# Performance work log

Measured on AMD Instinct MI355X. Metric: run time of the kernel, lower is better.

Reference implementation:

```python
import jax, jax.numpy as jnp
import numpy as np

ORDER = 2  # kernel_size


def setup_inputs() -> dict:
    key = jax.random.key(0)
    ks = jax.random.split(key, 8)
    B, F, N, T, H = 8, 1, 1024, 128, 64
    c_in = (ORDER * 2 + 1) * (2 * F + H)  # 330
    x = jax.random.normal(ks[0], (B, F, N, T), jnp.float32)
    mask = jax.random.randint(ks[1], (B, F, N, T), 0, 2).astype(jnp.bool_)
    adj = jax.random.uniform(ks[2], (N, N), jnp.float32)
    Wr = jax.random.normal(ks[3], (H, c_in), jnp.float32) * 0.05
    Wu = jax.random.normal(ks[4], (H, c_in), jnp.float32) * 0.05
    Wc = jax.random.normal(ks[5], (H, c_in), jnp.float32) * 0.05
    Wout = jax.random.normal(ks[6], (F, H), jnp.float32) * 0.05
    return {"x": x, "mask": mask, "adj": adj,
            "Wr": Wr, "br": jnp.zeros((H,), jnp.float32),
            "Wu": Wu, "bu": jnp.zeros((H,), jnp.float32),
            "Wc": Wc, "bc": jnp.zeros((H,), jnp.float32),
            "Wout": Wout, "bout": jnp.zeros((F,), jnp.float32)}


def reference(x, mask, adj, Wr, br, Wu, bu, Wc, bc, Wout, bout):
    # compute_support: forward/backward row-normalized diffusion matrices
    sup_f = adj / (adj.sum(1, keepdims=True) + 1e-8)
    adj_t = adj.T
    sup_b = adj_t / (adj_t.sum(1, keepdims=True) + 1e-8)
    supports = (sup_f, sup_b)

    def sconv(z, W, b):  # SpatialConvOrderK, z: [B,C,N]
        outs = [z]
        for a in supports:
            z1 = z
            for _ in range(ORDER):
                z1 = jnp.einsum('bcv,wv->bcw', z1, a)
                outs.append(z1)
        zc = jnp.concatenate(outs, axis=1)  # [B, 5*C, N]
        return jnp.einsum('bcn,oc->bon', zc, W) + b[None, :, None]

    def cell(inp, h):  # GCGRUCell
        xh = jnp.concatenate([inp, h], axis=1)
        r = jax.nn.sigmoid(sconv(xh, Wr, br))
        u = jax.nn.sigmoid(sconv(xh, Wu, bu))
        c = jnp.tanh(sconv(jnp.concatenate([inp, r * h], axis=1), Wc, bc))
        return u * h + (1.0 - u) * c

    B, F, N, T = x.shape
    H = Wout.shape[1]
    h0 = jnp.zeros((B, H, N), x.dtype)  # n_nodes=None -> zero init
    xs = jnp.moveaxis(x, -1, 0)    # [T,B,F,N]
    ms = jnp.moveaxis(mask, -1, 0)

    def step(h, xm):
        x_s, m_s = xm
        x_hat = jnp.einsum('bhn,oh->bon', h, Wout) + bout[None, :, None]
        state = h[None]  # n_layers=1 -> [L,B,H,N]
        x_in = jnp.where(m_s, x_s, x_hat)
        inp = jnp.concatenate([x_in, m_s.astype(x_s.dtype)], axis=1)
        return cell(inp, h), (x_hat, state)

    _, (preds, states) = jax.lax.scan(step, h0, (xs, ms))
    predictions = jnp.moveaxis(preds, 0, -1)  # [B,F,N,T]
    states = jnp.moveaxis(states, 0, -1)      # [L,B,H,N,T]
    return predictions, states
```

## Files before the change

kernel.cpp:

```cpp
#include <hip/hip_runtime.h>
#include <math.h>


typedef unsigned short u16;
typedef unsigned int u32;
typedef short bf16x8 __attribute__((ext_vector_type(8)));
typedef float f32x4 __attribute__((ext_vector_type(4)));

#define MFMA16(a, b, c) __builtin_amdgcn_mfma_f32_16x16x32_bf16((a), (b), (c), 0, 0, 0)

#define Bz 8
#define Nn 1024
#define Tt 128
#define Hh 64
#define KC 416
#define CP 80

static __device__ __forceinline__ u16 f2b(float f) {
  u32 u = __float_as_uint(f);
  u = (u + 0x7FFFu + ((u >> 16) & 1u)) >> 16;
  return (u16)u;
}
static __device__ __forceinline__ float b2f(u16 s) { return __uint_as_float(((u32)s) << 16); }
static __device__ __forceinline__ bf16x8 ld8(const u16* p) { return *reinterpret_cast<const bf16x8*>(p); }
static __device__ __forceinline__ void st2f(u16* p, float a, float b) {
  *reinterpret_cast<u32*>(p) = (u32)f2b(a) | ((u32)f2b(b) << 16);
}
static __device__ __forceinline__ void st2u(u16* p, u16 a, u16 b) {
  *reinterpret_cast<u32*>(p) = (u32)a | ((u32)b << 16);
}
static __device__ __forceinline__ float sigm(float x) { return 1.f / (1.f + __expf(-x)); }
static __device__ __forceinline__ float tanh_f(float x) {
  x = fminf(fmaxf(x, -15.f), 15.f);
  float e = __expf(2.f * x);
  return (e - 1.f) / (e + 1.f);
}

__global__ __launch_bounds__(256) void ksums(const float* adj, float* rinv, float* cinv) {
  int id = blockIdx.x * 256 + threadIdx.x;
  if (id < 1024) {
    int w = id;
    float s = 0.f;
    for (int v = 0; v < 1024; ++v) s += adj[v * 1024 + w];
    cinv[w] = 1.f / (s + 1e-8f);
  } else {
    int w = id - 1024;
    float s = 0.f;
    for (int v = 0; v < 1024; ++v) s += adj[w * 1024 + v];
    rinv[w] = 1.f / (s + 1e-8f);
  }
}

__global__ __launch_bounds__(256) void kmakeops(const float* adj, const float* rinv, const float* cinv,
                                                u16* Aops, u16* supft, u16* supbt) {
  int idx = blockIdx.x * 256 + threadIdx.x;
  int w = idx >> 10, v = idx & 1023;
  float a = adj[idx];
  u16 f = f2b(a * rinv[w]);
  u16 bb = f2b(a * cinv[v]);
  Aops[idx] = f;
  supft[v * 1024 + w] = f;
  supbt[idx] = bb;
  Aops[2 * 1048576 + v * 1024 + w] = bb;
}

__global__ __launch_bounds__(256) void kA2(u16* Aops, const u16* supft, const u16* supbt) {
  int wg = blockIdx.x;
  int o2 = wg & 1, mt = (wg >> 1) & 7, ntt = (wg >> 4) & 7;
  const u16* Ab = Aops + (o2 ? 2 * 1048576 : 0);
  const u16* Bb = o2 ? supbt : supft;
  u16* Ob = Aops + (o2 ? 3 * 1048576 : 1048576);
  int tid = threadIdx.x, wave = tid >> 6, lane = tid & 63, l15 = lane & 15, quad = lane >> 4;
  int mbase = mt * 128 + wave * 32;
  f32x4 acc[2][8];
#pragma unroll
  for (int m = 0; m < 2; ++m)
#pragma unroll
    for (int j = 0; j < 8; ++j) acc[m][j] = (f32x4){0.f, 0.f, 0.f, 0.f};
  for (int k = 0; k < 1024; k += 32) {
    int kq = k + quad * 8;
    bf16x8 av[2], bv[8];
#pragma unroll
    for (int m = 0; m < 2; ++m) av[m] = ld8(Ab + (mbase + m * 16 + l15) * 1024 + kq);
#pragma unroll
    for (int j = 0; j < 8; ++j) bv[j] = ld8(Bb + (ntt * 128 + j * 16 + l15) * 1024 + kq);
#pragma unroll
    for (int m = 0; m < 2; ++m)
#pragma unroll
      for (int j = 0; j < 8; ++j) acc[m][j] = MFMA16(av[m], bv[j], acc[m][j]);
  }
#pragma unroll
  for (int m = 0; m < 2; ++m)
#pragma unroll
    for (int j = 0; j < 8; ++j) {
      int v = ntt * 128 + j * 16 + l15;
#pragma unroll
      for (int i = 0; i < 4; ++i) {
        int w = mbase + m * 16 + quad * 4 + i;
        Ob[w * 1024 + v] = f2b(acc[m][j][i]);
      }
    }
}

__global__ __launch_bounds__(256) void kpackw(const float* Wr, const float* Wu, const float* Wc,
                                              u16* Wrup, u16* Wcp) {
  int idx = blockIdx.x * 256 + threadIdx.x;
  int r = idx / KC, k = idx % KC;
  float wv = 0.f;
  if (k < 396) {
    int c = (k < 66) ? k : (k - 66);
    if (r < 64) wv = Wr[r * 330 + c];
    else if (r < 128) wv = Wu[(r - 64) * 330 + c];
    else wv = Wc[(r - 128) * 330 + c];
  }
  if (r < 128) Wrup[r * KC + k] = f2b(wv);
  else Wcp[(r - 128) * KC + k] = f2b(wv);
}

__global__ __launch_bounds__(256) void kstep0(const float* x, const int* mask, const float* bout,
                                              float* h, float* states, float* preds,
                                              u16* xh, u16* xc, u16* zct, u16* yct) {
  int idx = blockIdx.x * 256 + threadIdx.x;
  int b = idx >> 16, o = (idx >> 10) & 63, n = idx & 1023;
  int hidx = (b * 64 + o) * 1024 + n;
  h[hidx] = 0.f;
  states[hidx * 128] = 0.f;
  xh[(b * CP + 2 + o) * 1024 + n] = 0;
  zct[(b * 1024 + n) * KC + 2 + o] = 0;
  zct[(b * 1024 + n) * KC + 68 + o] = 0;
  if (o == 0) {
    int xi = (b * 1024 + n) * 128;
    float xhat = bout[0];
    int mv = mask[xi];
    float xin = mv ? x[xi] : xhat;
    preds[xi] = xhat;
    u16 hi = f2b(xin), lo = f2b(xin - b2f(hi));
    xh[(b * CP + 0) * 1024 + n] = hi;
    xh[(b * CP + 1) * 1024 + n] = f2b((float)mv);
    u16* zr = zct + (b * 1024 + n) * KC;
    zr[0] = hi; zr[1] = f2b((float)mv); zr[66] = lo; zr[67] = 0;
  } else if (o == 1) {
    for (int j = 66; j < 80; ++j) {
      xh[(b * CP + j) * 1024 + n] = 0;
      xc[(b * CP + j) * 1024 + n] = 0;
    }
    u16* zr = zct + (b * 1024 + n) * KC;
    u16* yr = yct + (b * 1024 + n) * KC;
    for (int j = 396; j < KC; ++j) { zr[j] = 0; yr[j] = 0; }
  }
}

__global__ __launch_bounds__(256) void kdiff(const u16* __restrict__ Zin, const u16* __restrict__ Aops,
                                             u16* __restrict__ outT) {
  int wg = blockIdx.x;
  int nth = wg & 1, op = (wg >> 1) & 3, ntl = (wg >> 3) & 3, b = (wg >> 5) & 7;
  int nt = nth * 4 + ntl;
  int tid = threadIdx.x, wave = tid >> 6, lane = tid & 63, l15 = lane & 15, quad = lane >> 4;
  const u16* Zb = Zin + b * CP * 1024;
  const u16* Ab = Aops + op * 1048576;
  int colbase = nt * 128 + wave * 32;
  f32x4 acc[5][2];
#pragma unroll
  for (int m = 0; m < 5; ++m)
#pragma unroll
    for (int j = 0; j < 2; ++j) acc[m][j] = (f32x4){0.f, 0.f, 0.f, 0.f};
  for (int k = 0; k < 1024; k += 32) {
    int kq = k + quad * 8;
    bf16x8 av[5], bv[2];
#pragma unroll
    for (int m = 0; m < 5; ++m) av[m] = ld8(Zb + (m * 16 + l15) * 1024 + kq);
#pragma unroll
    for (int j = 0; j < 2; ++j) bv[j] = ld8(Ab + (colbase + j * 16 + l15) * 1024 + kq);
#pragma unroll
    for (int m = 0; m < 5; ++m)
#pragma unroll
      for (int j = 0; j < 2; ++j) acc[m][j] = MFMA16(av[m], bv[j], acc[m][j]);
  }
  int cbase = 132 + op * 66;
#pragma unroll
  for (int j = 0; j < 2; ++j) {
    int w = colbase + j * 16 + l15;
    u16* orow = outT + (b * 1024 + w) * KC + cbase;
#pragma unroll
    for (int m = 0; m < 5; ++m) {
      int c0 = m * 16 + quad * 4;
      if (c0 < 64) {
        st2f(orow + c0, acc[m][j][0], acc[m][j][1]);
        st2f(orow + c0 + 2, acc[m][j][2], acc[m][j][3]);
      } else if (c0 == 64) {
        st2f(orow + 64, acc[m][j][0], acc[m][j][1]);
      }
    }
  }
}

__global__ __launch_bounds__(256) void kconv_ru(const u16* __restrict__ zct, const u16* __restrict__ Wrup,
                                                const float* br, const float* bu,
                                                const float* __restrict__ h, float* __restrict__ ubuf,
                                                u16* __restrict__ xc, u16* __restrict__ yct) {
  int wg = blockIdx.x;
  int b = wg >> 5, nt = wg & 31;
  int tid = threadIdx.x, wave = tid >> 6, lane = tid & 63, l15 = lane & 15, quad = lane >> 4;
  int obase = wave * 32;
  f32x4 acc[2][2];
#pragma unroll
  for (int m = 0; m < 2; ++m)
#pragma unroll
    for (int j = 0; j < 2; ++j) acc[m][j] = (f32x4){0.f, 0.f, 0.f, 0.f};
  for (int k = 0; k < KC; k += 32) {
    int kq = k + quad * 8;
    bf16x8 av[2], bv[2];
#pragma unroll
    for (int m = 0; m < 2; ++m) av[m] = ld8(Wrup + (obase + m * 16 + l15) * KC + kq);
#pragma unroll
    for (int j = 0; j < 2; ++j) bv[j] = ld8(zct + ((b * 1024 + nt * 32 + j * 16 + l15) * KC + kq));
#pragma unroll
    for (int m = 0; m < 2; ++m)
#pragma unroll
      for (int j = 0; j < 2; ++j) acc[m][j] = MFMA16(av[m], bv[j], acc[m][j]);
  }
#pragma unroll
  for (int m = 0; m < 2; ++m)
#pragma unroll
    for (int j = 0; j < 2; ++j) {
      int o0 = obase + m * 16 + quad * 4;
      int n = nt * 32 + j * 16 + l15;
      if (o0 < 64) {
        u16 hi[4], lo[4];
#pragma unroll
        for (int i = 0; i < 4; ++i) {
          float s = sigm(acc[m][j][i] + br[o0 + i]);
          float rh = s * h[(b * 64 + o0 + i) * 1024 + n];
          hi[i] = f2b(rh);
          lo[i] = f2b(rh - b2f(hi[i]));
          xc[(b * CP + 2 + o0 + i) * 1024 + n] = hi[i];
        }
        u16* yr = yct + (b * 1024 + n) * KC;
        st2u(yr + 2 + o0, hi[0], hi[1]);
        st2u(yr + 4 + o0, hi[2], hi[3]);
        st2u(yr + 68 + o0, lo[0], lo[1]);
        st2u(yr + 70 + o0, lo[2], lo[3]);
      } else {
#pragma unroll
        for (int i = 0; i < 4; ++i)
          ubuf[(b * 64 + o0 - 64 + i) * 1024 + n] = sigm(acc[m][j][i] + bu[o0 - 64 + i]);
      }
    }
  if (tid < 32) {
    int n = nt * 32 + tid;
    const u16* zr = zct + (b * 1024 + n) * KC;
    u16* yr = yct + (b * 1024 + n) * KC;
    yr[0] = zr[0]; yr[1] = zr[1]; yr[66] = zr[66]; yr[67] = zr[67];
    xc[(b * CP + 0) * 1024 + n] = zr[0];
    xc[(b * CP + 1) * 1024 + n] = zr[1];
  }
}

__global__ __launch_bounds__(256) void kconv_c(const u16* __restrict__ yct, const u16* __restrict__ Wcp,
                                               const float* bc, const float* __restrict__ ubuf,
                                               float* __restrict__ h, const float* __restrict__ x,
                                               const int* __restrict__ mask, const float* Wout,
                                               const float* bout, float* __restrict__ preds,
                                               float* __restrict__ states, u16* __restrict__ xh,
                                               u16* __restrict__ zct, int t) {
  __shared__ float lds[64 * 65];
  int wg = blockIdx.x;
  int b = wg >> 4, nt = wg & 15;
  int tid = threadIdx.x, wave = tid >> 6, lane = tid & 63, l15 = lane & 15, quad = lane >> 4;
  int nl = wave * 16 + l15;
  int n = nt * 64 + nl;
  f32x4 acc[4];
#pragma unroll
  for (int m = 0; m < 4; ++m) acc[m] = (f32x4){0.f, 0.f, 0.f, 0.f};
  for (int k = 0; k < KC; k += 32) {
    int kq = k + quad * 8;
    bf16x8 bv = ld8(yct + (b * 1024 + n) * KC + kq);
#pragma unroll
    for (int m = 0; m < 4; ++m) {
      bf16x8 av = ld8(Wcp + (m * 16 + l15) * KC + kq);
      acc[m] = MFMA16(av, bv, acc[m]);
    }
  }
  int t1 = t + 1;
#pragma unroll
  for (int m = 0; m < 4; ++m) {
    int o0 = m * 16 + quad * 4;
    u16 hi[4], lo[4];
#pragma unroll
    for (int i = 0; i < 4; ++i) {
      int o = o0 + i;
      float c = tanh_f(acc[m][i] + bc[o]);
      int idx = (b * 64 + o) * 1024 + n;
      float u = ubuf[idx], hp = h[idx];
      float hn = u * hp + (1.f - u) * c;
      h[idx] = hn;
      lds[o * 65 + nl] = hn;
      hi[i] = f2b(hn);
      lo[i] = f2b(hn - b2f(hi[i]));
      if (t1 < Tt) {
        states[idx * 128 + t1] = hn;
        xh[(b * CP + 2 + o) * 1024 + n] = hi[i];
      }
    }
    if (t1 < Tt) {
      u16* zr = zct + (b * 1024 + n) * KC;
      st2u(zr + 2 + o0, hi[0], hi[1]);
      st2u(zr + 4 + o0, hi[2], hi[3]);
      st2u(zr + 68 + o0, lo[0], lo[1]);
      st2u(zr + 70 + o0, lo[2], lo[3]);
    }
  }
  __syncthreads();
  if (tid < 64 && t1 < Tt) {
    int nn = nt * 64 + tid;
    float xhat = bout[0];
    for (int o = 0; o < 64; ++o) xhat += Wout[o] * lds[o * 65 + tid];
    int xi = (b * 1024 + nn) * 128 + t1;
    int mv = mask[xi];
    float xin = mv ? x[xi] : xhat;
    preds[xi] = xhat;
    u16 hi = f2b(xin), lo = f2b(xin - b2f(hi));
    xh[(b * CP + 0) * 1024 + nn] = hi;
    xh[(b * CP + 1) * 1024 + nn] = f2b((float)mv);
    u16* zr = zct + (b * 1024 + nn) * KC;
    zr[0] = hi; zr[1] = f2b((float)mv); zr[66] = lo; zr[67] = 0;
  }
}

extern "C" void kernel_launch(void* const* d_in, const int* in_sizes, int n_in,
                              void* d_out, int out_size, void* d_ws, size_t ws_size,
                              hipStream_t stream) {
  const float* x = (const float*)d_in[0];
  const int* mask = (const int*)d_in[1];
  const float* adj = (const float*)d_in[2];
  const float* Wr = (const float*)d_in[3];
  const float* br = (const float*)d_in[4];
  const float* Wu = (const float*)d_in[5];
  const float* bu = (const float*)d_in[6];
  const float* Wc = (const float*)d_in[7];
  const float* bc = (const float*)d_in[8];
  const float* Wout = (const float*)d_in[9];
  const float* bout = (const float*)d_in[10];

  float* preds = (float*)d_out;
  float* states = preds + 8 * 1024 * 128;

  u16* Aops = (u16*)d_ws;
  u16* supft = Aops + 4 * 1048576;
  u16* supbt = supft + 1048576;
  float* rinv = (float*)(supbt + 1048576);
  float* cinv = rinv + 1024;
  u16* xh = (u16*)(cinv + 1024);
  u16* xc = xh + Bz * CP * 1024;
  u16* zct = xc + Bz * CP * 1024;
  u16* yct = zct + Bz * 1024 * KC;
  u16* Wrup = yct + Bz * 1024 * KC;
  u16* Wcp = Wrup + 128 * KC;
  float* ubuf = (float*)(Wcp + 64 * KC);
  float* h = ubuf + Bz * 64 * 1024;

  ksums<<<8, 256, 0, stream>>>(adj, rinv, cinv);
  kmakeops<<<4096, 256, 0, stream>>>(adj, rinv, cinv, Aops, supft, supbt);
  kA2<<<128, 256, 0, stream>>>(Aops, supft, supbt);
  kpackw<<<312, 256, 0, stream>>>(Wr, Wu, Wc, Wrup, Wcp);
  kstep0<<<2048, 256, 0, stream>>>(x, mask, bout, h, states, preds, xh, xc, zct, yct);

  for (int t = 0; t < Tt; ++t) {
    kdiff<<<256, 256, 0, stream>>>(xh, Aops, zct);
    kconv_ru<<<256, 256, 0, stream>>>(zct, Wrup, br, bu, h, ubuf, xc, yct);
    kdiff<<<256, 256, 0, stream>>>(xc, Aops, yct);
    kconv_c<<<128, 256, 0, stream>>>(yct, Wcp, bc, ubuf, h, x, mask, Wout, bout,
                                     preds, states, xh, zct, t);
  }
}
```

Baseline: 12.42 ms.

## Fuse diffusion GEMMs into gate-conv kernels via shared-memory staging

Merges each diffusion kernel with the following gate convolution (kdiff+kconv_ru into kphA, kdiff+kconv_c into kphB). Each 16-node tile computes the four diffusion outputs into LDS and then runs the weight GEMM from LDS, so the per-step launch count drops from four to two. The global z/y buffers shrink to a 136-wide stride that holds only the raw and hidden columns. In exchange, each block redundantly re-reads the full xh/xc operand for every 16-column tile, and the per-wave MFMA reuse is smaller.

```diff
diff --git a/kernel.cpp b/kernel.cpp
--- a/kernel.cpp
+++ b/kernel.cpp
@@ -10,10 +10,11 @@
 #define MFMA16(a, b, c) __builtin_amdgcn_mfma_f32_16x16x32_bf16((a), (b), (c), 0, 0, 0)
 
 #define Bz 8
-#define Nn 1024
 #define Tt 128
 #define Hh 64
 #define KC 416
+#define KD 136
+#define KL 424
 #define CP 80
 
 static __device__ __forceinline__ u16 f2b(float f) {
@@ -106,6 +107,7 @@
                                               u16* Wrup, u16* Wcp) {
   int idx = blockIdx.x * 256 + threadIdx.x;
   int r = idx / KC, k = idx % KC;
+  if (r >= 192) return;
   float wv = 0.f;
   if (k < 396) {
     int c = (k < 66) ? k : (k - 66);
@@ -119,15 +121,16 @@
 
 __global__ __launch_bounds__(256) void kstep0(const float* x, const int* mask, const float* bout,
                                               float* h, float* states, float* preds,
-                                              u16* xh, u16* xc, u16* zct, u16* yct) {
+                                              u16* xh, u16* xc, u16* zct) {
   int idx = blockIdx.x * 256 + threadIdx.x;
   int b = idx >> 16, o = (idx >> 10) & 63, n = idx & 1023;
   int hidx = (b * 64 + o) * 1024 + n;
   h[hidx] = 0.f;
-  states[hidx * 128] = 0.f;
+  states[(size_t)hidx * 128] = 0.f;
   xh[(b * CP + 2 + o) * 1024 + n] = 0;
-  zct[(b * 1024 + n) * KC + 2 + o] = 0;
-  zct[(b * 1024 + n) * KC + 68 + o] = 0;
+  u16* zr = zct + (size_t)(b * 1024 + n) * KD;
+  zr[2 + o] = 0;
+  zr[68 + o] = 0;
   if (o == 0) {
     int xi = (b * 1024 + n) * 128;
     float xhat = bout[0];
@@ -137,105 +140,88 @@
     u16 hi = f2b(xin), lo = f2b(xin - b2f(hi));
     xh[(b * CP + 0) * 1024 + n] = hi;
     xh[(b * CP + 1) * 1024 + n] = f2b((float)mv);
-    u16* zr = zct + (b * 1024 + n) * KC;
     zr[0] = hi; zr[1] = f2b((float)mv); zr[66] = lo; zr[67] = 0;
   } else if (o == 1) {
     for (int j = 66; j < 80; ++j) {
       xh[(b * CP + j) * 1024 + n] = 0;
       xc[(b * CP + j) * 1024 + n] = 0;
     }
-    u16* zr = zct + (b * 1024 + n) * KC;
-    u16* yr = yct + (b * 1024 + n) * KC;
-    for (int j = 396; j < KC; ++j) { zr[j] = 0; yr[j] = 0; }
-  }
-}
-
-__global__ __launch_bounds__(256) void kdiff(const u16* __restrict__ Zin, const u16* __restrict__ Aops,
-                                             u16* __restrict__ outT) {
+  }
+}
+
+__global__ __launch_bounds__(256) void kphA(const u16* __restrict__ xh, const u16* __restrict__ Aops,
+                                            const u16* __restrict__ zct, const u16* __restrict__ Wrup,
+                                            const float* br, const float* bu,
+                                            const float* __restrict__ h, float* __restrict__ ubuf,
+                                            u16* __restrict__ xc, u16* __restrict__ yct) {
+  __shared__ u16 zl[16][KL];
   int wg = blockIdx.x;
-  int nth = wg & 1, op = (wg >> 1) & 3, ntl = (wg >> 3) & 3, b = (wg >> 5) & 7;
-  int nt = nth * 4 + ntl;
+  int b = wg >> 6, nt = wg & 63;
   int tid = threadIdx.x, wave = tid >> 6, lane = tid & 63, l15 = lane & 15, quad = lane >> 4;
-  const u16* Zb = Zin + b * CP * 1024;
-  const u16* Ab = Aops + op * 1048576;
-  int colbase = nt * 128 + wave * 32;
-  f32x4 acc[5][2];
-#pragma unroll
-  for (int m = 0; m < 5; ++m)
-#pragma unroll
-    for (int j = 0; j < 2; ++j) acc[m][j] = (f32x4){0.f, 0.f, 0.f, 0.f};
-  for (int k = 0; k < 1024; k += 32) {
-    int kq = k + quad * 8;
-    bf16x8 av[5], bv[2];
-#pragma unroll
-    for (int m = 0; m < 5; ++m) av[m] = ld8(Zb + (m * 16 + l15) * 1024 + kq);
-#pragma unroll
-    for (int j = 0; j < 2; ++j) bv[j] = ld8(Ab + (colbase + j * 16 + l15) * 1024 + kq);
-#pragma unroll
-    for (int m = 0; m < 5; ++m)
-#pragma unroll
-      for (int j = 0; j < 2; ++j) acc[m][j] = MFMA16(av[m], bv[j], acc[m][j]);
-  }
-  int cbase = 132 + op * 66;
-#pragma unroll
-  for (int j = 0; j < 2; ++j) {
-    int w = colbase + j * 16 + l15;
-    u16* orow = outT + (b * 1024 + w) * KC + cbase;
+  for (int i = tid; i < 16 * 76; i += 256) {
+    int n = i / 76, c = i - n * 76;
+    u32* dst = (u32*)zl[n];
+    if (c < 66) dst[c] = ((const u32*)(zct + (size_t)(b * 1024 + nt * 16 + n) * KD))[c];
+    else dst[132 + c] = 0;
+  }
+  {
+    const u16* Zb = xh + b * CP * 1024;
+    const u16* Ab = Aops + (wave << 20);
+    int col = nt * 16 + l15;
+    f32x4 acc[5];
+#pragma unroll
+    for (int m = 0; m < 5; ++m) acc[m] = (f32x4){0.f, 0.f, 0.f, 0.f};
+    for (int k = 0; k < 1024; k += 32) {
+      int kq = k + quad * 8;
+      bf16x8 bv = ld8(Ab + col * 1024 + kq);
+      bf16x8 av[5];
+#pragma unroll
+      for (int m = 0; m < 5; ++m) av[m] = ld8(Zb + (m * 16 + l15) * 1024 + kq);
+#pragma unroll
+      for (int m = 0; m < 5; ++m) acc[m] = MFMA16(av[m], bv, acc[m]);
+    }
+    int cbase = 132 + wave * 66;
+    u16* orow = zl[l15] + cbase;
 #pragma unroll
     for (int m = 0; m < 5; ++m) {
       int c0 = m * 16 + quad * 4;
       if (c0 < 64) {
-        st2f(orow + c0, acc[m][j][0], acc[m][j][1]);
-        st2f(orow + c0 + 2, acc[m][j][2], acc[m][j][3]);
+        st2f(orow + c0, acc[m][0], acc[m][1]);
+        st2f(orow + c0 + 2, acc[m][2], acc[m][3]);
       } else if (c0 == 64) {
-        st2f(orow + 64, acc[m][j][0], acc[m][j][1]);
+        st2f(orow + 64, acc[m][0], acc[m][1]);
       }
     }
   }
-}
-
-__global__ __launch_bounds__(256) void kconv_ru(const u16* __restrict__ zct, const u16* __restrict__ Wrup,
-                                                const float* br, const float* bu,
-                                                const float* __restrict__ h, float* __restrict__ ubuf,
-                                                u16* __restrict__ xc, u16* __restrict__ yct) {
-  int wg = blockIdx.x;
-  int b = wg >> 5, nt = wg & 31;
-  int tid = threadIdx.x, wave = tid >> 6, lane = tid & 63, l15 = lane & 15, quad = lane >> 4;
-  int obase = wave * 32;
-  f32x4 acc[2][2];
-#pragma unroll
-  for (int m = 0; m < 2; ++m)
-#pragma unroll
-    for (int j = 0; j < 2; ++j) acc[m][j] = (f32x4){0.f, 0.f, 0.f, 0.f};
-  for (int k = 0; k < KC; k += 32) {
-    int kq = k + quad * 8;
-    bf16x8 av[2], bv[2];
-#pragma unroll
-    for (int m = 0; m < 2; ++m) av[m] = ld8(Wrup + (obase + m * 16 + l15) * KC + kq);
-#pragma unroll
-    for (int j = 0; j < 2; ++j) bv[j] = ld8(zct + ((b * 1024 + nt * 32 + j * 16 + l15) * KC + kq));
-#pragma unroll
-    for (int m = 0; m < 2; ++m)
-#pragma unroll
-      for (int j = 0; j < 2; ++j) acc[m][j] = MFMA16(av[m], bv[j], acc[m][j]);
-  }
-#pragma unroll
-  for (int m = 0; m < 2; ++m)
-#pragma unroll
-    for (int j = 0; j < 2; ++j) {
+  __syncthreads();
+  {
+    int obase = wave * 32;
+    f32x4 acc[2];
+    acc[0] = (f32x4){0.f, 0.f, 0.f, 0.f};
+    acc[1] = (f32x4){0.f, 0.f, 0.f, 0.f};
+    for (int k = 0; k < KC; k += 32) {
+      int kq = k + quad * 8;
+      bf16x8 bv = ld8(zl[l15] + kq);
+      bf16x8 av0 = ld8(Wrup + (obase + l15) * KC + kq);
+      bf16x8 av1 = ld8(Wrup + (obase + 16 + l15) * KC + kq);
+      acc[0] = MFMA16(av0, bv, acc[0]);
+      acc[1] = MFMA16(av1, bv, acc[1]);
+    }
+    int n = nt * 16 + l15;
+#pragma unroll
+    for (int m = 0; m < 2; ++m) {
       int o0 = obase + m * 16 + quad * 4;
-      int n = nt * 32 + j * 16 + l15;
       if (o0 < 64) {
         u16 hi[4], lo[4];
 #pragma unroll
         for (int i = 0; i < 4; ++i) {
-          float s = sigm(acc[m][j][i] + br[o0 + i]);
+          float s = sigm(acc[m][i] + br[o0 + i]);
           float rh = s * h[(b * 64 + o0 + i) * 1024 + n];
           hi[i] = f2b(rh);
           lo[i] = f2b(rh - b2f(hi[i]));
           xc[(b * CP + 2 + o0 + i) * 1024 + n] = hi[i];
         }
-        u16* yr = yct + (b * 1024 + n) * KC;
+        u16* yr = yct + (size_t)(b * 1024 + n) * KD;
         st2u(yr + 2 + o0, hi[0], hi[1]);
         st2u(yr + 4 + o0, hi[2], hi[3]);
         st2u(yr + 68 + o0, lo[0], lo[1]);
@@ -243,87 +229,118 @@
       } else {
 #pragma unroll
         for (int i = 0; i < 4; ++i)
-          ubuf[(b * 64 + o0 - 64 + i) * 1024 + n] = sigm(acc[m][j][i] + bu[o0 - 64 + i]);
+          ubuf[(b * 64 + o0 - 64 + i) * 1024 + n] = sigm(acc[m][i] + bu[o0 - 64 + i]);
       }
     }
-  if (tid < 32) {
-    int n = nt * 32 + tid;
-    const u16* zr = zct + (b * 1024 + n) * KC;
-    u16* yr = yct + (b * 1024 + n) * KC;
+  }
+  if (tid < 16) {
+    int n = nt * 16 + tid;
+    const u16* zr = zl[tid];
+    u16* yr = yct + (size_t)(b * 1024 + n) * KD;
     yr[0] = zr[0]; yr[1] = zr[1]; yr[66] = zr[66]; yr[67] = zr[67];
     xc[(b * CP + 0) * 1024 + n] = zr[0];
     xc[(b * CP + 1) * 1024 + n] = zr[1];
   }
 }
 
-__global__ __launch_bounds__(256) void kconv_c(const u16* __restrict__ yct, const u16* __restrict__ Wcp,
-                                               const float* bc, const float* __restrict__ ubuf,
-                                               float* __restrict__ h, const float* __restrict__ x,
-                                               const int* __restrict__ mask, const float* Wout,
-                                               const float* bout, float* __restrict__ preds,
-                                               float* __restrict__ states, u16* __restrict__ xh,
-                                               u16* __restrict__ zct, int t) {
-  __shared__ float lds[64 * 65];
+__global__ __launch_bounds__(256) void kphB(const u16* __restrict__ xc, const u16* __restrict__ Aops,
+                                            const u16* __restrict__ yct, const u16* __restrict__ Wcp,
+                                            const float* bc, const float* __restrict__ ubuf,
+                                            float* __restrict__ h, const float* __restrict__ x,
+                                            const int* __restrict__ mask, const float* Wout,
+                                            const float* bout, float* __restrict__ preds,
+                                            float* __restrict__ states, u16* __restrict__ xh,
+                                            u16* __restrict__ zct, int t) {
+  __shared__ u16 yl[16][KL];
+  __shared__ float hbuf[64][17];
   int wg = blockIdx.x;
-  int b = wg >> 4, nt = wg & 15;
+  int b = wg >> 6, nt = wg & 63;
   int tid = threadIdx.x, wave = tid >> 6, lane = tid & 63, l15 = lane & 15, quad = lane >> 4;
-  int nl = wave * 16 + l15;
-  int n = nt * 64 + nl;
-  f32x4 acc[4];
-#pragma unroll
-  for (int m = 0; m < 4; ++m) acc[m] = (f32x4){0.f, 0.f, 0.f, 0.f};
+  for (int i = tid; i < 16 * 76; i += 256) {
+    int n = i / 76, c = i - n * 76;
+    u32* dst = (u32*)yl[n];
+    if (c < 66) dst[c] = ((const u32*)(yct + (size_t)(b * 1024 + nt * 16 + n) * KD))[c];
+    else dst[132 + c] = 0;
+  }
+  {
+    const u16* Zb = xc + b * CP * 1024;
+    const u16* Ab = Aops + (wave << 20);
+    int col = nt * 16 + l15;
+    f32x4 acc[5];
+#pragma unroll
+    for (int m = 0; m < 5; ++m) acc[m] = (f32x4){0.f, 0.f, 0.f, 0.f};
+    for (int k = 0; k < 1024; k += 32) {
+      int kq = k + quad * 8;
+      bf16x8 bv = ld8(Ab + col * 1024 + kq);
+      bf16x8 av[5];
+#pragma unroll
+      for (int m = 0; m < 5; ++m) av[m] = ld8(Zb + (m * 16 + l15) * 1024 + kq);
+#pragma unroll
+      for (int m = 0; m < 5; ++m) acc[m] = MFMA16(av[m], bv, acc[m]);
+    }
+    int cbase = 132 + wave * 66;
+    u16* orow = yl[l15] + cbase;
+#pragma unroll
+    for (int m = 0; m < 5; ++m) {
+      int c0 = m * 16 + quad * 4;
+      if (c0 < 64) {
+        st2f(orow + c0, acc[m][0], acc[m][1]);
+        st2f(orow + c0 + 2, acc[m][2], acc[m][3]);
+      } else if (c0 == 64) {
+        st2f(orow + 64, acc[m][0], acc[m][1]);
+      }
+    }
+  }
+  __syncthreads();
+  f32x4 acc = (f32x4){0.f, 0.f, 0.f, 0.f};
   for (int k = 0; k < KC; k += 32) {
     int kq = k + quad * 8;
-    bf16x8 bv = ld8(yct + (b * 1024 + n) * KC + kq);
-#pragma unroll
-    for (int m = 0; m < 4; ++m) {
-      bf16x8 av = ld8(Wcp + (m * 16 + l15) * KC + kq);
-      acc[m] = MFMA16(av, bv, acc[m]);
-    }
+    bf16x8 bv = ld8(yl[l15] + kq);
+    bf16x8 av = ld8(Wcp + (wave * 16 + l15) * KC + kq);
+    acc = MFMA16(av, bv, acc);
   }
   int t1 = t + 1;
-#pragma unroll
-  for (int m = 0; m < 4; ++m) {
-    int o0 = m * 16 + quad * 4;
-    u16 hi[4], lo[4];
-#pragma unroll
-    for (int i = 0; i < 4; ++i) {
-      int o = o0 + i;
-      float c = tanh_f(acc[m][i] + bc[o]);
-      int idx = (b * 64 + o) * 1024 + n;
-      float u = ubuf[idx], hp = h[idx];
-      float hn = u * hp + (1.f - u) * c;
-      h[idx] = hn;
-      lds[o * 65 + nl] = hn;
-      hi[i] = f2b(hn);
-      lo[i] = f2b(hn - b2f(hi[i]));
-      if (t1 < Tt) {
-        states[idx * 128 + t1] = hn;
-        xh[(b * CP + 2 + o) * 1024 + n] = hi[i];
-      }
-    }
+  int n = nt * 16 + l15;
+  int o0 = wave * 16 + quad * 4;
+  u16 hi[4], lo[4];
+#pragma unroll
+  for (int i = 0; i < 4; ++i) {
+    int o = o0 + i;
+    float c = tanh_f(acc[i] + bc[o]);
+    int idx = (b * 64 + o) * 1024 + n;
+    float u = ubuf[idx], hp = h[idx];
+    float hn = u * hp + (1.f - u) * c;
+    h[idx] = hn;
+    hbuf[o][l15] = hn;
+    hi[i] = f2b(hn);
+    lo[i] = f2b(hn - b2f(hi[i]));
     if (t1 < Tt) {
-      u16* zr = zct + (b * 1024 + n) * KC;
-      st2u(zr + 2 + o0, hi[0], hi[1]);
-      st2u(zr + 4 + o0, hi[2], hi[3]);
-      st2u(zr + 68 + o0, lo[0], lo[1]);
-      st2u(zr + 70 + o0, lo[2], lo[3]);
-    }
+      states[(size_t)idx * 128 + t1] = hn;
+      xh[(b * CP + 2 + o) * 1024 + n] = hi[i];
+    }
+  }
+  if (t1 < Tt) {
+    u16* zr = zct + (size_t)(b * 1024 + n) * KD;
+    st2u(zr + 2 + o0, hi[0], hi[1]);
+    st2u(zr + 4 + o0, hi[2], hi[3]);
+    st2u(zr + 68 + o0, lo[0], lo[1]);
+    st2u(zr + 70 + o0, lo[2], lo[3]);
   }
   __syncthreads();
-  if (tid < 64 && t1 < Tt) {
-    int nn = nt * 64 + tid;
+  if (tid < 16 && t1 < Tt) {
+    int nn = nt * 16 + tid;
     float xhat = bout[0];
-    for (int o = 0; o < 64; ++o) xhat += Wout[o] * lds[o * 65 + tid];
+#pragma unroll
+    for (int o = 0; o < 64; ++o) xhat += Wout[o] * hbuf[o][tid];
     int xi = (b * 1024 + nn) * 128 + t1;
     int mv = mask[xi];
     float xin = mv ? x[xi] : xhat;
     preds[xi] = xhat;
-    u16 hi = f2b(xin), lo = f2b(xin - b2f(hi));
-    xh[(b * CP + 0) * 1024 + nn] = hi;
+    u16 hi2 = f2b(xin), lo2 = f2b(xin - b2f(hi2));
+    xh[(b * CP + 0) * 1024 + nn] = hi2;
     xh[(b * CP + 1) * 1024 + nn] = f2b((float)mv);
-    u16* zr = zct + (b * 1024 + nn) * KC;
-    zr[0] = hi; zr[1] = f2b((float)mv); zr[66] = lo; zr[67] = 0;
+    u16* zr = zct + (size_t)(b * 1024 + nn) * KD;
+    zr[0] = hi2; zr[1] = f2b((float)mv); zr[66] = lo2; zr[67] = 0;
   }
 }
 
@@ -353,8 +370,8 @@
   u16* xh = (u16*)(cinv + 1024);
   u16* xc = xh + Bz * CP * 1024;
   u16* zct = xc + Bz * CP * 1024;
-  u16* yct = zct + Bz * 1024 * KC;
-  u16* Wrup = yct + Bz * 1024 * KC;
+  u16* yct = zct + Bz * 1024 * KD;
+  u16* Wrup = yct + Bz * 1024 * KD;
   u16* Wcp = Wrup + 128 * KC;
   float* ubuf = (float*)(Wcp + 64 * KC);
   float* h = ubuf + Bz * 64 * 1024;
@@ -363,13 +380,11 @@
   kmakeops<<<4096, 256, 0, stream>>>(adj, rinv, cinv, Aops, supft, supbt);
   kA2<<<128, 256, 0, stream>>>(Aops, supft, supbt);
   kpackw<<<312, 256, 0, stream>>>(Wr, Wu, Wc, Wrup, Wcp);
-  kstep0<<<2048, 256, 0, stream>>>(x, mask, bout, h, states, preds, xh, xc, zct, yct);
+  kstep0<<<2048, 256, 0, stream>>>(x, mask, bout, h, states, preds, xh, xc, zct);
 
   for (int t = 0; t < Tt; ++t) {
-    kdiff<<<256, 256, 0, stream>>>(xh, Aops, zct);
-    kconv_ru<<<256, 256, 0, stream>>>(zct, Wrup, br, bu, h, ubuf, xc, yct);
-    kdiff<<<256, 256, 0, stream>>>(xc, Aops, yct);
-    kconv_c<<<128, 256, 0, stream>>>(yct, Wcp, bc, ubuf, h, x, mask, Wout, bout,
-                                     preds, states, xh, zct, t);
-  }
-}
+    kphA<<<512, 256, 0, stream>>>(xh, Aops, zct, Wrup, br, bu, h, ubuf, xc, yct);
+    kphB<<<512, 256, 0, stream>>>(xc, Aops, yct, Wcp, bc, ubuf, h, x, mask, Wout, bout,
+                                  preds, states, xh, zct, t);
+  }
+}
```

Result: slower. 14.07 ms (+13.3%).

## Fuse diffusion GEMM with gate convolution into two kernels per step via LDS

Applied to the files above, without the earlier changes.

Each timestep's diffusion matmul and following gate convolution are merged into one kernel: diffusion results are written into a shared-memory concat tile instead of the global zct/yct buffers, then consumed directly by the gate GEMM. This halves per-step launches from four to two and removes the global round-trip of the large transposed concat buffers. Both GEMMs use split-K across two wave halves with an LDS reduction. The hi/lo bf16 split channels now live as extra rows in xh/xc (CP raised to 148). The cost is heavier LDS use and extra syncs, which limits each block to one per CU.

```diff
diff --git a/kernel.cpp b/kernel.cpp
--- a/kernel.cpp
+++ b/kernel.cpp
@@ -10,11 +10,13 @@
 #define MFMA16(a, b, c) __builtin_amdgcn_mfma_f32_16x16x32_bf16((a), (b), (c), 0, 0, 0)
 
 #define Bz 8
-#define Nn 1024
 #define Tt 128
 #define Hh 64
 #define KC 416
-#define CP 80
+#define KL 424
+#define CP 148
+#define ZLB (32 * KL * 2)
+#define SCRB (4 * 64 * 44 * 4)
 
 static __device__ __forceinline__ u16 f2b(float f) {
   u32 u = __float_as_uint(f);
@@ -25,9 +27,6 @@
 static __device__ __forceinline__ bf16x8 ld8(const u16* p) { return *reinterpret_cast<const bf16x8*>(p); }
 static __device__ __forceinline__ void st2f(u16* p, float a, float b) {
   *reinterpret_cast<u32*>(p) = (u32)f2b(a) | ((u32)f2b(b) << 16);
-}
-static __device__ __forceinline__ void st2u(u16* p, u16 a, u16 b) {
-  *reinterpret_cast<u32*>(p) = (u32)a | ((u32)b << 16);
 }
 static __device__ __forceinline__ float sigm(float x) { return 1.f / (1.f + __expf(-x)); }
 static __device__ __forceinline__ float tanh_f(float x) {
@@ -106,6 +105,7 @@
                                               u16* Wrup, u16* Wcp) {
   int idx = blockIdx.x * 256 + threadIdx.x;
   int r = idx / KC, k = idx % KC;
+  if (r >= 192) return;
   float wv = 0.f;
   if (k < 396) {
     int c = (k < 66) ? k : (k - 66);
@@ -119,211 +119,309 @@
 
 __global__ __launch_bounds__(256) void kstep0(const float* x, const int* mask, const float* bout,
                                               float* h, float* states, float* preds,
-                                              u16* xh, u16* xc, u16* zct, u16* yct) {
-  int idx = blockIdx.x * 256 + threadIdx.x;
-  int b = idx >> 16, o = (idx >> 10) & 63, n = idx & 1023;
-  int hidx = (b * 64 + o) * 1024 + n;
-  h[hidx] = 0.f;
-  states[hidx * 128] = 0.f;
-  xh[(b * CP + 2 + o) * 1024 + n] = 0;
-  zct[(b * 1024 + n) * KC + 2 + o] = 0;
-  zct[(b * 1024 + n) * KC + 68 + o] = 0;
-  if (o == 0) {
-    int xi = (b * 1024 + n) * 128;
-    float xhat = bout[0];
-    int mv = mask[xi];
-    float xin = mv ? x[xi] : xhat;
-    preds[xi] = xhat;
-    u16 hi = f2b(xin), lo = f2b(xin - b2f(hi));
-    xh[(b * CP + 0) * 1024 + n] = hi;
-    xh[(b * CP + 1) * 1024 + n] = f2b((float)mv);
-    u16* zr = zct + (b * 1024 + n) * KC;
-    zr[0] = hi; zr[1] = f2b((float)mv); zr[66] = lo; zr[67] = 0;
-  } else if (o == 1) {
-    for (int j = 66; j < 80; ++j) {
-      xh[(b * CP + j) * 1024 + n] = 0;
-      xc[(b * CP + j) * 1024 + n] = 0;
-    }
-    u16* zr = zct + (b * 1024 + n) * KC;
-    u16* yr = yct + (b * 1024 + n) * KC;
-    for (int j = 396; j < KC; ++j) { zr[j] = 0; yr[j] = 0; }
-  }
-}
-
-__global__ __launch_bounds__(256) void kdiff(const u16* __restrict__ Zin, const u16* __restrict__ Aops,
-                                             u16* __restrict__ outT) {
+                                              u16* xh, u16* xc) {
   int wg = blockIdx.x;
-  int nth = wg & 1, op = (wg >> 1) & 3, ntl = (wg >> 3) & 3, b = (wg >> 5) & 7;
-  int nt = nth * 4 + ntl;
-  int tid = threadIdx.x, wave = tid >> 6, lane = tid & 63, l15 = lane & 15, quad = lane >> 4;
-  const u16* Zb = Zin + b * CP * 1024;
-  const u16* Ab = Aops + op * 1048576;
-  int colbase = nt * 128 + wave * 32;
-  f32x4 acc[5][2];
-#pragma unroll
-  for (int m = 0; m < 5; ++m)
-#pragma unroll
-    for (int j = 0; j < 2; ++j) acc[m][j] = (f32x4){0.f, 0.f, 0.f, 0.f};
-  for (int k = 0; k < 1024; k += 32) {
-    int kq = k + quad * 8;
-    bf16x8 av[5], bv[2];
-#pragma unroll
-    for (int m = 0; m < 5; ++m) av[m] = ld8(Zb + (m * 16 + l15) * 1024 + kq);
-#pragma unroll
-    for (int j = 0; j < 2; ++j) bv[j] = ld8(Ab + (colbase + j * 16 + l15) * 1024 + kq);
-#pragma unroll
-    for (int m = 0; m < 5; ++m)
-#pragma unroll
-      for (int j = 0; j < 2; ++j) acc[m][j] = MFMA16(av[m], bv[j], acc[m][j]);
-  }
-  int cbase = 132 + op * 66;
-#pragma unroll
-  for (int j = 0; j < 2; ++j) {
-    int w = colbase + j * 16 + l15;
-    u16* orow = outT + (b * 1024 + w) * KC + cbase;
-#pragma unroll
-    for (int m = 0; m < 5; ++m) {
-      int c0 = m * 16 + quad * 4;
-      if (c0 < 64) {
-        st2f(orow + c0, acc[m][j][0], acc[m][j][1]);
-        st2f(orow + c0 + 2, acc[m][j][2], acc[m][j][3]);
-      } else if (c0 == 64) {
-        st2f(orow + 64, acc[m][j][0], acc[m][j][1]);
-      }
-    }
-  }
-}
-
-__global__ __launch_bounds__(256) void kconv_ru(const u16* __restrict__ zct, const u16* __restrict__ Wrup,
-                                                const float* br, const float* bu,
-                                                const float* __restrict__ h, float* __restrict__ ubuf,
-                                                u16* __restrict__ xc, u16* __restrict__ yct) {
+  int b = wg / 148, row = wg - b * 148;
+  int n = threadIdx.x * 4;
+  for (int k = 0; k < 4; ++k, ++n) {
+    u16 xhv = 0;
+    if (row == 0 || row == 1 || row == 80) {
+      int xi = (b * 1024 + n) * 128;
+      int mv = mask[xi];
+      float xhat = bout[0];
+      float xin = mv ? x[xi] : xhat;
+      u16 hi = f2b(xin);
+      if (row == 0) { xhv = hi; preds[xi] = xhat; }
+      else if (row == 1) xhv = f2b((float)mv);
+      else xhv = f2b(xin - b2f(hi));
+    }
+    xh[(b * CP + row) * 1024 + n] = xhv;
+    xc[(b * CP + row) * 1024 + n] = 0;
+    if (row >= 2 && row < 66) {
+      int o = row - 2;
+      int idx = (b * 64 + o) * 1024 + n;
+      h[idx] = 0.f;
+      states[(size_t)idx * 128] = 0.f;
+    }
+  }
+}
+
+__global__ __launch_bounds__(512, 1) void kphA(const u16* __restrict__ xh, const u16* __restrict__ Aops,
+                                               const u16* __restrict__ Wrup,
+                                               const float* br, const float* bu,
+                                               const float* __restrict__ h, float* __restrict__ ubuf,
+                                               u16* __restrict__ xc) {
+  extern __shared__ char smem[];
+  u16 (*zl)[KL] = (u16(*)[KL])smem;
+  float* scr = (float*)(smem + ZLB);
   int wg = blockIdx.x;
   int b = wg >> 5, nt = wg & 31;
-  int tid = threadIdx.x, wave = tid >> 6, lane = tid & 63, l15 = lane & 15, quad = lane >> 4;
-  int obase = wave * 32;
-  f32x4 acc[2][2];
+  int n0 = nt * 32;
+  int tid = threadIdx.x, w = tid >> 6, lane = tid & 63, l15 = lane & 15, quad = lane >> 4;
+  int op = w & 3, kh = w >> 2;
+
+  for (int i = tid; i < 2112; i += 512) {
+    int ch = i >> 4, cp = i & 15;
+    int srow = ch < 66 ? ch : ch + 14;
+    u32 v = *(const u32*)(xh + (b * CP + srow) * 1024 + n0 + cp * 2);
+    zl[cp * 2][ch] = (u16)v;
+    zl[cp * 2 + 1][ch] = (u16)(v >> 16);
+    if (ch == 0 || ch == 1 || ch == 66 || ch == 67)
+      *(u32*)(xc + (b * CP + srow) * 1024 + n0 + cp * 2) = v;
+  }
+  for (int i = tid; i < 320; i += 512) {
+    int n = i / 10, c = i - n * 10;
+    ((u32*)zl[n])[198 + c] = 0;
+  }
+
+  f32x4 dacc[5][2];
+#pragma unroll
+  for (int m = 0; m < 5; ++m)
+#pragma unroll
+    for (int j = 0; j < 2; ++j) dacc[m][j] = (f32x4){0.f, 0.f, 0.f, 0.f};
+  {
+    const u16* Zb = xh + b * CP * 1024;
+    const u16* Ab = Aops + (op << 20);
+    int kbase = kh << 9;
+    for (int k = 0; k < 512; k += 32) {
+      int kq = kbase + k + quad * 8;
+      bf16x8 av[5], bv[2];
+#pragma unroll
+      for (int m = 0; m < 5; ++m) av[m] = ld8(Zb + (m * 16 + l15) * 1024 + kq);
+#pragma unroll
+      for (int j = 0; j < 2; ++j) bv[j] = ld8(Ab + (n0 + j * 16 + l15) * 1024 + kq);
+#pragma unroll
+      for (int m = 0; m < 5; ++m)
+#pragma unroll
+        for (int j = 0; j < 2; ++j) dacc[m][j] = MFMA16(av[m], bv[j], dacc[m][j]);
+    }
+  }
+  if (kh) {
+    f32x4* s = (f32x4*)(scr + (op * 64 + lane) * 44);
+#pragma unroll
+    for (int m = 0; m < 5; ++m)
+#pragma unroll
+      for (int j = 0; j < 2; ++j) s[m * 2 + j] = dacc[m][j];
+  }
+  __syncthreads();
+  if (!kh) {
+    f32x4* s = (f32x4*)(scr + (op * 64 + lane) * 44);
+    int cbase = 132 + op * 66;
+#pragma unroll
+    for (int m = 0; m < 5; ++m)
+#pragma unroll
+      for (int j = 0; j < 2; ++j) {
+        f32x4 a = dacc[m][j] + s[m * 2 + j];
+        u16* orow = zl[j * 16 + l15] + cbase;
+        int c0 = m * 16 + quad * 4;
+        if (c0 < 64) {
+          st2f(orow + c0, a[0], a[1]);
+          st2f(orow + c0 + 2, a[2], a[3]);
+        } else if (c0 == 64) {
+          st2f(orow + 64, a[0], a[1]);
+        }
+      }
+  }
+  __syncthreads();
+
+  int og = w & 3, obase = og * 32;
+  f32x4 cacc[2][2];
 #pragma unroll
   for (int m = 0; m < 2; ++m)
 #pragma unroll
-    for (int j = 0; j < 2; ++j) acc[m][j] = (f32x4){0.f, 0.f, 0.f, 0.f};
-  for (int k = 0; k < KC; k += 32) {
-    int kq = k + quad * 8;
-    bf16x8 av[2], bv[2];
-#pragma unroll
-    for (int m = 0; m < 2; ++m) av[m] = ld8(Wrup + (obase + m * 16 + l15) * KC + kq);
-#pragma unroll
-    for (int j = 0; j < 2; ++j) bv[j] = ld8(zct + ((b * 1024 + nt * 32 + j * 16 + l15) * KC + kq));
+    for (int j = 0; j < 2; ++j) cacc[m][j] = (f32x4){0.f, 0.f, 0.f, 0.f};
+  {
+    int k0 = kh ? 224 : 0, k1 = kh ? KC : 224;
+    for (int k = k0; k < k1; k += 32) {
+      int kq = k + quad * 8;
+      bf16x8 av[2], bv[2];
+#pragma unroll
+      for (int m = 0; m < 2; ++m) av[m] = ld8(Wrup + (obase + m * 16 + l15) * KC + kq);
+#pragma unroll
+      for (int j = 0; j < 2; ++j) bv[j] = ld8(zl[j * 16 + l15] + kq);
+#pragma unroll
+      for (int m = 0; m < 2; ++m)
+#pragma unroll
+        for (int j = 0; j < 2; ++j) cacc[m][j] = MFMA16(av[m], bv[j], cacc[m][j]);
+    }
+  }
+  if (kh) {
+    f32x4* s = (f32x4*)(scr + (og * 64 + lane) * 44);
 #pragma unroll
     for (int m = 0; m < 2; ++m)
 #pragma unroll
-      for (int j = 0; j < 2; ++j) acc[m][j] = MFMA16(av[m], bv[j], acc[m][j]);
-  }
-#pragma unroll
-  for (int m = 0; m < 2; ++m)
-#pragma unroll
-    for (int j = 0; j < 2; ++j) {
-      int o0 = obase + m * 16 + quad * 4;
-      int n = nt * 32 + j * 16 + l15;
-      if (o0 < 64) {
-        u16 hi[4], lo[4];
-#pragma unroll
-        for (int i = 0; i < 4; ++i) {
-          float s = sigm(acc[m][j][i] + br[o0 + i]);
-          float rh = s * h[(b * 64 + o0 + i) * 1024 + n];
-          hi[i] = f2b(rh);
-          lo[i] = f2b(rh - b2f(hi[i]));
-          xc[(b * CP + 2 + o0 + i) * 1024 + n] = hi[i];
+      for (int j = 0; j < 2; ++j) s[m * 2 + j] = cacc[m][j];
+  }
+  __syncthreads();
+  if (!kh) {
+    f32x4* s = (f32x4*)(scr + (og * 64 + lane) * 44);
+#pragma unroll
+    for (int m = 0; m < 2; ++m)
+#pragma unroll
+      for (int j = 0; j < 2; ++j) {
+        f32x4 a = cacc[m][j] + s[m * 2 + j];
+        int o0 = obase + m * 16 + quad * 4;
+        int n = n0 + j * 16 + l15;
+        if (o0 < 64) {
+#pragma unroll
+          for (int i = 0; i < 4; ++i) {
+            float sg = sigm(a[i] + br[o0 + i]);
+            float rh = sg * h[(b * 64 + o0 + i) * 1024 + n];
+            u16 hi = f2b(rh);
+            xc[(b * CP + 2 + o0 + i) * 1024 + n] = hi;
+            xc[(b * CP + 82 + o0 + i) * 1024 + n] = f2b(rh - b2f(hi));
+          }
+        } else {
+#pragma unroll
+          for (int i = 0; i < 4; ++i)
+            ubuf[(b * 64 + o0 - 64 + i) * 1024 + n] = sigm(a[i] + bu[o0 - 64 + i]);
         }
-        u16* yr = yct + (b * 1024 + n) * KC;
-        st2u(yr + 2 + o0, hi[0], hi[1]);
-        st2u(yr + 4 + o0, hi[2], hi[3]);
-        st2u(yr + 68 + o0, lo[0], lo[1]);
-        st2u(yr + 70 + o0, lo[2], lo[3]);
-      } else {
-#pragma unroll
-        for (int i = 0; i < 4; ++i)
-          ubuf[(b * 64 + o0 - 64 + i) * 1024 + n] = sigm(acc[m][j][i] + bu[o0 - 64 + i]);
       }
-    }
-  if (tid < 32) {
-    int n = nt * 32 + tid;
-    const u16* zr = zct + (b * 1024 + n) * KC;
-    u16* yr = yct + (b * 1024 + n) * KC;
-    yr[0] = zr[0]; yr[1] = zr[1]; yr[66] = zr[66]; yr[67] = zr[67];
-    xc[(b * CP + 0) * 1024 + n] = zr[0];
-    xc[(b * CP + 1) * 1024 + n] = zr[1];
-  }
-}
-
-__global__ __launch_bounds__(256) void kconv_c(const u16* __restrict__ yct, const u16* __restrict__ Wcp,
+  }
+}
+
+__global__ __launch_bounds__(512, 1) void kphB(const u16* __restrict__ xc, const u16* __restrict__ Aops,
+                                               const u16* __restrict__ Wcp,
                                                const float* bc, const float* __restrict__ ubuf,
                                                float* __restrict__ h, const float* __restrict__ x,
                                                const int* __restrict__ mask, const float* Wout,
                                                const float* bout, float* __restrict__ preds,
                                                float* __restrict__ states, u16* __restrict__ xh,
-                                               u16* __restrict__ zct, int t) {
-  __shared__ float lds[64 * 65];
+                                               int t) {
+  extern __shared__ char smem[];
+  u16 (*yl)[KL] = (u16(*)[KL])smem;
+  float* scr = (float*)(smem + ZLB);
+  float* hbuf = (float*)(smem + ZLB + SCRB);
   int wg = blockIdx.x;
-  int b = wg >> 4, nt = wg & 15;
-  int tid = threadIdx.x, wave = tid >> 6, lane = tid & 63, l15 = lane & 15, quad = lane >> 4;
-  int nl = wave * 16 + l15;
-  int n = nt * 64 + nl;
-  f32x4 acc[4];
-#pragma unroll
-  for (int m = 0; m < 4; ++m) acc[m] = (f32x4){0.f, 0.f, 0.f, 0.f};
-  for (int k = 0; k < KC; k += 32) {
-    int kq = k + quad * 8;
-    bf16x8 bv = ld8(yct + (b * 1024 + n) * KC + kq);
-#pragma unroll
-    for (int m = 0; m < 4; ++m) {
-      bf16x8 av = ld8(Wcp + (m * 16 + l15) * KC + kq);
-      acc[m] = MFMA16(av, bv, acc[m]);
-    }
-  }
+  int b = wg >> 5, nt = wg & 31;
+  int n0 = nt * 32;
+  int tid = threadIdx.x, w = tid >> 6, lane = tid & 63, l15 = lane & 15, quad = lane >> 4;
+  int op = w & 3, kh = w >> 2;
+
+  for (int i = tid; i < 2112; i += 512) {
+    int ch = i >> 4, cp = i & 15;
+    int srow = ch < 66 ? ch : ch + 14;
+    u32 v = *(const u32*)(xc + (b * CP + srow) * 1024 + n0 + cp * 2);
+    yl[cp * 2][ch] = (u16)v;
+    yl[cp * 2 + 1][ch] = (u16)(v >> 16);
+  }
+  for (int i = tid; i < 320; i += 512) {
+    int n = i / 10, c = i - n * 10;
+    ((u32*)yl[n])[198 + c] = 0;
+  }
+
+  f32x4 dacc[5][2];
+#pragma unroll
+  for (int m = 0; m < 5; ++m)
+#pragma unroll
+    for (int j = 0; j < 2; ++j) dacc[m][j] = (f32x4){0.f, 0.f, 0.f, 0.f};
+  {
+    const u16* Zb = xc + b * CP * 1024;
+    const u16* Ab = Aops + (op << 20);
+    int kbase = kh << 9;
+    for (int k = 0; k < 512; k += 32) {
+      int kq = kbase + k + quad * 8;
+      bf16x8 av[5], bv[2];
+#pragma unroll
+      for (int m = 0; m < 5; ++m) av[m] = ld8(Zb + (m * 16 + l15) * 1024 + kq);
+#pragma unroll
+      for (int j = 0; j < 2; ++j) bv[j] = ld8(Ab + (n0 + j * 16 + l15) * 1024 + kq);
+#pragma unroll
+      for (int m = 0; m < 5; ++m)
+#pragma unroll
+        for (int j = 0; j < 2; ++j) dacc[m][j] = MFMA16(av[m], bv[j], dacc[m][j]);
+    }
+  }
+  if (kh) {
+    f32x4* s = (f32x4*)(scr + (op * 64 + lane) * 44);
+#pragma unroll
+    for (int m = 0; m < 5; ++m)
+#pragma unroll
+      for (int j = 0; j < 2; ++j) s[m * 2 + j] = dacc[m][j];
+  }
+  __syncthreads();
+  if (!kh) {
+    f32x4* s = (f32x4*)(scr + (op * 64 + lane) * 44);
+    int cbase = 132 + op * 66;
+#pragma unroll
+    for (int m = 0; m < 5; ++m)
+#pragma unroll
+      for (int j = 0; j < 2; ++j) {
+        f32x4 a = dacc[m][j] + s[m * 2 + j];
+        u16* orow = yl[j * 16 + l15] + cbase;
+        int c0 = m * 16 + quad * 4;
+        if (c0 < 64) {
+          st2f(orow + c0, a[0], a[1]);
+          st2f(orow + c0 + 2, a[2], a[3]);
+        } else if (c0 == 64) {
+          st2f(orow + 64, a[0], a[1]);
+        }
+      }
+  }
+  __syncthreads();
+
+  int og = w & 1, jg = (w >> 1) & 1, task = w & 3;
+  int obase = og * 32;
+  f32x4 cacc[2];
+  cacc[0] = (f32x4){0.f, 0.f, 0.f, 0.f};
+  cacc[1] = (f32x4){0.f, 0.f, 0.f, 0.f};
+  {
+    int k0 = kh ? 224 : 0, k1 = kh ? KC : 224;
+    for (int k = k0; k < k1; k += 32) {
+      int kq = k + quad * 8;
+      bf16x8 bv = ld8(yl[jg * 16 + l15] + kq);
+      bf16x8 av0 = ld8(Wcp + (obase + l15) * KC + kq);
+      bf16x8 av1 = ld8(Wcp + (obase + 16 + l15) * KC + kq);
+      cacc[0] = MFMA16(av0, bv, cacc[0]);
+      cacc[1] = MFMA16(av1, bv, cacc[1]);
+    }
+  }
+  if (kh) {
+    f32x4* s = (f32x4*)(scr + (task * 64 + lane) * 44);
+    s[0] = cacc[0];
+    s[1] = cacc[1];
+  }
+  __syncthreads();
   int t1 = t + 1;
-#pragma unroll
-  for (int m = 0; m < 4; ++m) {
-    int o0 = m * 16 + quad * 4;
-    u16 hi[4], lo[4];
-#pragma unroll
-    for (int i = 0; i < 4; ++i) {
-      int o = o0 + i;
-      float c = tanh_f(acc[m][i] + bc[o]);
-      int idx = (b * 64 + o) * 1024 + n;
-      float u = ubuf[idx], hp = h[idx];
-      float hn = u * hp + (1.f - u) * c;
-      h[idx] = hn;
-      lds[o * 65 + nl] = hn;
-      hi[i] = f2b(hn);
-      lo[i] = f2b(hn - b2f(hi[i]));
-      if (t1 < Tt) {
-        states[idx * 128 + t1] = hn;
-        xh[(b * CP + 2 + o) * 1024 + n] = hi[i];
+  if (!kh) {
+    f32x4* s = (f32x4*)(scr + (task * 64 + lane) * 44);
+    int n = n0 + jg * 16 + l15, nloc = jg * 16 + l15;
+#pragma unroll
+    for (int m = 0; m < 2; ++m) {
+      f32x4 a = cacc[m] + s[m];
+      int o0 = obase + m * 16 + quad * 4;
+#pragma unroll
+      for (int i = 0; i < 4; ++i) {
+        int o = o0 + i;
+        float c = tanh_f(a[i] + bc[o]);
+        int idx = (b * 64 + o) * 1024 + n;
+        float u = ubuf[idx], hp = h[idx];
+        float hn = u * hp + (1.f - u) * c;
+        h[idx] = hn;
+        hbuf[o * 33 + nloc] = hn;
+        u16 hi = f2b(hn);
+        if (t1 < Tt) {
+          states[(size_t)idx * 128 + t1] = hn;
+          xh[(b * CP + 2 + o) * 1024 + n] = hi;
+          xh[(b * CP + 82 + o) * 1024 + n] = f2b(hn - b2f(hi));
+        }
       }
     }
-    if (t1 < Tt) {
-      u16* zr = zct + (b * 1024 + n) * KC;
-      st2u(zr + 2 + o0, hi[0], hi[1]);
-      st2u(zr + 4 + o0, hi[2], hi[3]);
-      st2u(zr + 68 + o0, lo[0], lo[1]);
-      st2u(zr + 70 + o0, lo[2], lo[3]);
-    }
-  }
-  __syncthreads();
-  if (tid < 64 && t1 < Tt) {
-    int nn = nt * 64 + tid;
+  }
+  __syncthreads();
+  if (tid < 32 && t1 < Tt) {
+    int nn = n0 + tid;
     float xhat = bout[0];
-    for (int o = 0; o < 64; ++o) xhat += Wout[o] * lds[o * 65 + tid];
+#pragma unroll
+    for (int o = 0; o < 64; ++o) xhat += Wout[o] * hbuf[o * 33 + tid];
     int xi = (b * 1024 + nn) * 128 + t1;
     int mv = mask[xi];
     float xin = mv ? x[xi] : xhat;
     preds[xi] = xhat;
-    u16 hi = f2b(xin), lo = f2b(xin - b2f(hi));
-    xh[(b * CP + 0) * 1024 + nn] = hi;
+    u16 hi2 = f2b(xin);
+    xh[(b * CP + 0) * 1024 + nn] = hi2;
     xh[(b * CP + 1) * 1024 + nn] = f2b((float)mv);
-    u16* zr = zct + (b * 1024 + nn) * KC;
-    zr[0] = hi; zr[1] = f2b((float)mv); zr[66] = lo; zr[67] = 0;
+    xh[(b * CP + 80) * 1024 + nn] = f2b(xin - b2f(hi2));
   }
 }
 
@@ -352,24 +450,28 @@
   float* cinv = rinv + 1024;
   u16* xh = (u16*)(cinv + 1024);
   u16* xc = xh + Bz * CP * 1024;
-  u16* zct = xc + Bz * CP * 1024;
-  u16* yct = zct + Bz * 1024 * KC;
-  u16* Wrup = yct + Bz * 1024 * KC;
+  u16* Wrup = xc + Bz * CP * 1024;
   u16* Wcp = Wrup + 128 * KC;
   float* ubuf = (float*)(Wcp + 64 * KC);
   float* h = ubuf + Bz * 64 * 1024;
+
+  static int lds_set = 0;
+  if (!lds_set) {
+    hipFuncSetAttribute((const void*)kphA, hipFuncAttributeMaxDynamicSharedMemorySize, ZLB + SCRB);
+    hipFuncSetAttribute((const void*)kphB, hipFuncAttributeMaxDynamicSharedMemorySize,
+                        ZLB + SCRB + 64 * 33 * 4);
+    lds_set = 1;
+  }
 
   ksums<<<8, 256, 0, stream>>>(adj, rinv, cinv);
   kmakeops<<<4096, 256, 0, stream>>>(adj, rinv, cinv, Aops, supft, supbt);
   kA2<<<128, 256, 0, stream>>>(Aops, supft, supbt);
   kpackw<<<312, 256, 0, stream>>>(Wr, Wu, Wc, Wrup, Wcp);
-  kstep0<<<2048, 256, 0, stream>>>(x, mask, bout, h, states, preds, xh, xc, zct, yct);
+  kstep0<<<1184, 256, 0, stream>>>(x, mask, bout, h, states, preds, xh, xc);
 
   for (int t = 0; t < Tt; ++t) {
-    kdiff<<<256, 256, 0, stream>>>(xh, Aops, zct);
-    kconv_ru<<<256, 256, 0, stream>>>(zct, Wrup, br, bu, h, ubuf, xc, yct);
-    kdiff<<<256, 256, 0, stream>>>(xc, Aops, yct);
-    kconv_c<<<128, 256, 0, stream>>>(yct, Wcp, bc, ubuf, h, x, mask, Wout, bout,
-                                     preds, states, xh, zct, t);
-  }
-}
+    kphA<<<256, 512, ZLB + SCRB, stream>>>(xh, Aops, Wrup, br, bu, h, ubuf, xc);
+    kphB<<<256, 512, ZLB + SCRB + 64 * 33 * 4, stream>>>(xc, Aops, Wcp, bc, ubuf, h, x, mask,
+                                                         Wout, bout, preds, states, xh, t);
+  }
+}
```

Result: faster. 10.09 ms (-18.8%).
